# Kernel tuning notes

Hardware: AMD Instinct MI355X
Metric: run time of the kernel (lower is better)

Reference implementation:

```python
import jax, jax.numpy as jnp
import numpy as np

T = 16          # time_span
N = 128         # num_trajectory
D = 512         # embedding dim
TEMP = 0.1      # temperature
INF = 1000000000.0
M = 2 * N * T   # total rows of z (two views)


def setup_inputs() -> dict:
    key = jax.random.key(0)
    k1, k2 = jax.random.split(key)
    z = jax.random.normal(k1, (M, D), dtype=jnp.float32)
    done = jax.random.randint(k2, (T, N), 0, 2).astype(jnp.int32)  # [T, N] binary done flags
    return {"z": z, "done": done}


def _build_positive_mask(done):
    # done: [T, N] int -> transposed to [N, T] as in the torch code
    d = done.astype(jnp.float32).T  # [N, T]
    # Sequential rewrite loop is equivalent to:
    #   done_new[r,t] = 1 iff exists original done at p < t in row r AND orig done[r,t] == 0
    excl = jnp.cumsum(d, axis=1) - d  # exclusive cumsum along time
    d_new = jnp.where((excl > 0) & (d == 0), 1.0, 0.0)  # [N, T]
    done_vec = 1.0 - d_new.reshape(-1)  # [N*T]
    # block-diagonal temporal mask: same trajectory => 1
    traj = jnp.arange(N * T) // T
    block = (traj[:, None] == traj[None, :]).astype(jnp.float32)  # [NT, NT]
    done_mask = (done_vec[:, None] * done_vec[None, :]) * block
    done_mask = jnp.tile(done_mask, (2, 2))      # [M, M]
    temporal_mask = jnp.tile(block, (2, 2))      # [M, M]
    eye = jnp.eye(M, dtype=jnp.float32)
    positive_mask = (1.0 - done_mask) * (1.0 - temporal_mask) + eye
    return positive_mask, eye


def reference(z, done):
    positive_mask, eye = _build_positive_mask(done)
    # cosine similarity = normalize + GEMM (same math as broadcasted F.cosine_similarity)
    norms = jnp.maximum(jnp.linalg.norm(z, axis=-1, keepdims=True), 1e-8)
    zn = z / norms
    logits = (zn @ zn.T) / TEMP - eye * INF  # [M, M]
    log_probs = jax.nn.log_softmax(logits, axis=1)
    neg = 1.0 - positive_mask
    mean_log_prob = jnp.sum(neg * log_probs, axis=1) / jnp.sum(neg, axis=1)
    return -jnp.mean(mean_log_prob)
```

## Files before the change

### kernel.cpp

```cpp
#include <hip/hip_runtime.h>
#include <hip/hip_bf16.h>

typedef __bf16 bf16x8 __attribute__((ext_vector_type(8)));
typedef float f32x16 __attribute__((ext_vector_type(16)));
typedef unsigned int u32x4 __attribute__((ext_vector_type(4)));
typedef unsigned short u16;


__global__ void nrm_kernel(const float* __restrict__ z, u16* __restrict__ zn,
                           float* __restrict__ expsum, float* __restrict__ possum) {
    int row = blockIdx.x;
    int tid = threadIdx.x;
    float4 v = ((const float4*)(z + row * 512))[tid];
    float ss = v.x * v.x + v.y * v.y + v.z * v.z + v.w * v.w;
#pragma unroll
    for (int off = 32; off; off >>= 1) ss += __shfl_down(ss, off, 64);
    __shared__ float red[2];
    if ((tid & 63) == 0) red[tid >> 6] = ss;
    __syncthreads();
    float norm = fmaxf(sqrtf(red[0] + red[1]), 1e-8f);
    float sc = 1.0f / norm;
    __hip_bfloat16 b[4];
    b[0] = __float2bfloat16(v.x * sc);
    b[1] = __float2bfloat16(v.y * sc);
    b[2] = __float2bfloat16(v.z * sc);
    b[3] = __float2bfloat16(v.w * sc);
    uint2 p;
    __builtin_memcpy(&p, b, 8);
    ((uint2*)(zn + row * 512))[tid] = p;
    if (tid == 0) { expsum[row] = 0.f; possum[row] = 0.f; }
}

__global__ void pos_kernel(const u16* __restrict__ zn, float* __restrict__ possum) {
    int g = blockIdx.x;
    int l = threadIdx.x;
    int u = l & 31, h = l >> 5;
    int grow = (u < 16) ? (g * 16 + u) : (2048 + g * 16 + (u - 16));
    const u32x4* src = (const u32x4*)(zn + grow * 512);
    f32x16 acc = {};
#pragma unroll
    for (int kc = 0; kc < 32; ++kc) {
        bf16x8 f = __builtin_bit_cast(bf16x8, src[h + 2 * kc]);
        acc = __builtin_amdgcn_mfma_f32_32x32x16_bf16(f, f, acc, 0, 0, 0);
    }
#pragma unroll
    for (int r = 0; r < 16; ++r) {
        int rrow = (r & 3) + 8 * (r >> 2) + 4 * h;
        float v = (rrow == u) ? 0.f : acc[r];
        v += __shfl_xor(v, 1, 64);
        v += __shfl_xor(v, 2, 64);
        v += __shfl_xor(v, 4, 64);
        v += __shfl_xor(v, 8, 64);
        v += __shfl_xor(v, 16, 64);
        if (u == 0) {
            int gr = (rrow < 16) ? (g * 16 + rrow) : (2048 + g * 16 + (rrow - 16));
            possum[gr] = v * 10.0f;
        }
    }
}

__global__ __launch_bounds__(256, 2) void gemm_kernel(const u16* __restrict__ zn,
                                                      float* __restrict__ expsum) {
    __shared__ u16 Bt[32 * 520];
    int wave = threadIdx.x >> 6;
    int l = threadIdx.x & 63;
    int m = l & 31, h = l >> 5;
    int rowbase = blockIdx.x * 128 + wave * 32;
    int colchunk = blockIdx.y * 256;

    u32x4 a[32];
    const u32x4* arow = (const u32x4*)(zn + (rowbase + m) * 512);
#pragma unroll
    for (int kc = 0; kc < 32; ++kc) a[kc] = arow[h + 2 * kc];

    float expacc[16];
#pragma unroll
    for (int r = 0; r < 16; ++r) expacc[r] = 0.f;

    int c = threadIdx.x >> 3;
    int g0 = threadIdx.x & 7;

    for (int ct = 0; ct < 8; ++ct) {
        int colbase = colchunk + ct * 32;
        __syncthreads();
        const u32x4* src = (const u32x4*)(zn + (colbase + c) * 512);
        u32x4* dst = (u32x4*)(Bt + c * 520);
#pragma unroll
        for (int i = 0; i < 8; ++i) dst[g0 + 8 * i] = src[g0 + 8 * i];
        __syncthreads();

        f32x16 acc = {};
        const u32x4* brow = (const u32x4*)(Bt + m * 520);
#pragma unroll
        for (int kc = 0; kc < 32; ++kc) {
            bf16x8 bf = __builtin_bit_cast(bf16x8, brow[h + 2 * kc]);
            acc = __builtin_amdgcn_mfma_f32_32x32x16_bf16(
                __builtin_bit_cast(bf16x8, a[kc]), bf, acc, 0, 0, 0);
        }
        if (colbase == rowbase) {
#pragma unroll
            for (int r = 0; r < 16; ++r) {
                int rrow = (r & 3) + 8 * (r >> 2) + 4 * h;
                if (rrow != m) expacc[r] += __expf(acc[r] * 10.0f);
            }
        } else {
#pragma unroll
            for (int r = 0; r < 16; ++r) expacc[r] += __expf(acc[r] * 10.0f);
        }
    }
#pragma unroll
    for (int r = 0; r < 16; ++r) {
        float v = expacc[r];
        v += __shfl_xor(v, 1, 64);
        v += __shfl_xor(v, 2, 64);
        v += __shfl_xor(v, 4, 64);
        v += __shfl_xor(v, 8, 64);
        v += __shfl_xor(v, 16, 64);
        if (m == 0) {
            int rrow = (r & 3) + 8 * (r >> 2) + 4 * h;
            atomicAdd(&expsum[rowbase + rrow], v);
        }
    }
}

__global__ void fin_kernel(const float* __restrict__ expsum,
                           const float* __restrict__ possum, float* __restrict__ out) {
    int tid = threadIdx.x;
    float s = 0.f;
    for (int i = tid; i < 4096; i += 1024)
        s += __logf(expsum[i]) - possum[i] * (1.0f / 31.0f);
#pragma unroll
    for (int off = 32; off; off >>= 1) s += __shfl_down(s, off, 64);
    __shared__ float red[16];
    if ((tid & 63) == 0) red[tid >> 6] = s;
    __syncthreads();
    if (tid == 0) {
        float t = 0.f;
#pragma unroll
        for (int i = 0; i < 16; ++i) t += red[i];
        out[0] = t * (1.0f / 4096.0f);
    }
}

extern "C" void kernel_launch(void* const* d_in, const int* in_sizes, int n_in,
                              void* d_out, int out_size, void* d_ws, size_t ws_size,
                              hipStream_t stream) {
    const float* z = (const float*)d_in[0];
    u16* zn = (u16*)d_ws;
    float* expsum = (float*)((char*)d_ws + (4u << 20));
    float* possum = expsum + 4096;
    float* out = (float*)d_out;

    nrm_kernel<<<4096, 128, 0, stream>>>(z, zn, expsum, possum);
    pos_kernel<<<128, 64, 0, stream>>>(zn, possum);
    gemm_kernel<<<dim3(32, 16), 256, 0, stream>>>(zn, expsum);
    fin_kernel<<<1, 1024, 0, stream>>>(expsum, possum, out);
}
```

Measured before the change: 97.55 us.

## Exploit Gram symmetry with upper-triangular tiles and async double-buffered LDS loads

The GEMM now launches only the upper-triangular 128x128 block tiles (528 workgroups instead of 512 covering the full matrix, each with half the columns). Each off-diagonal tile contributes both row sums and column sums of exp(logits), with column sums added atomically. B tiles are streamed into a double-buffered, XOR-swizzled LDS buffer via global_load_lds async copies, and the K loop is split across two accumulators for more MFMA ILP. This roughly halves MFMA and exp work. In exchange it adds more atomics, per-block extra reduction work, and bf16 rounding that is now shared symmetrically.

After: 109.7 us. 1.12x slower.

```diff
diff --git a/kernel.cpp b/kernel.cpp
--- a/kernel.cpp
+++ b/kernel.cpp
@@ -6,6 +6,12 @@
 typedef unsigned int u32x4 __attribute__((ext_vector_type(4)));
 typedef unsigned short u16;
 
+
+__device__ inline void async_cp16(const u16* g, u16* l) {
+    __builtin_amdgcn_global_load_lds(
+        (const __attribute__((address_space(1))) unsigned int*)g,
+        (__attribute__((address_space(3))) unsigned int*)l, 16, 0, 0);
+}
 
 __global__ void nrm_kernel(const float* __restrict__ z, u16* __restrict__ zn,
                            float* __restrict__ expsum, float* __restrict__ possum) {
@@ -18,8 +24,7 @@
     __shared__ float red[2];
     if ((tid & 63) == 0) red[tid >> 6] = ss;
     __syncthreads();
-    float norm = fmaxf(sqrtf(red[0] + red[1]), 1e-8f);
-    float sc = 1.0f / norm;
+    float sc = 1.0f / fmaxf(sqrtf(red[0] + red[1]), 1e-8f);
     __hip_bfloat16 b[4];
     b[0] = __float2bfloat16(v.x * sc);
     b[1] = __float2bfloat16(v.y * sc);
@@ -61,15 +66,19 @@
 
 __global__ __launch_bounds__(256, 2) void gemm_kernel(const u16* __restrict__ zn,
                                                       float* __restrict__ expsum) {
-    __shared__ u16 Bt[32 * 520];
+    __shared__ u16 Bt[2][32 * 512];
     int wave = threadIdx.x >> 6;
     int l = threadIdx.x & 63;
     int m = l & 31, h = l >> 5;
-    int rowbase = blockIdx.x * 128 + wave * 32;
-    int colchunk = blockIdx.y * 256;
+
+    int t = blockIdx.x, i = 0;
+    while (t >= 32 - i) { t -= 32 - i; ++i; }
+    int j = i + t;
+    int rowbase = i * 128 + wave * 32;
+    bool diagwg = (i == j);
 
     u32x4 a[32];
-    const u32x4* arow = (const u32x4*)(zn + (rowbase + m) * 512);
+    const u32x4* arow = (const u32x4*)(zn + (size_t)(rowbase + m) * 512);
 #pragma unroll
     for (int kc = 0; kc < 32; ++kc) a[kc] = arow[h + 2 * kc];
 
@@ -77,35 +86,57 @@
 #pragma unroll
     for (int r = 0; r < 16; ++r) expacc[r] = 0.f;
 
-    int c = threadIdx.x >> 3;
-    int g0 = threadIdx.x & 7;
+    {
+        int colbase = j * 128;
+#pragma unroll
+        for (int it = 0; it < 8; ++it) {
+            int col = wave * 8 + it;
+            int s = col & 7;
+            async_cp16(zn + (size_t)(colbase + col) * 512 + ((l ^ s) * 8),
+                       &Bt[0][col * 512]);
+        }
+    }
 
-    for (int ct = 0; ct < 8; ++ct) {
-        int colbase = colchunk + ct * 32;
+    int sB = m & 7;
+    for (int ct = 0; ct < 4; ++ct) {
         __syncthreads();
-        const u32x4* src = (const u32x4*)(zn + (colbase + c) * 512);
-        u32x4* dst = (u32x4*)(Bt + c * 520);
+        if (ct < 3) {
+            int colbase = j * 128 + (ct + 1) * 32;
+            u16* dst = &Bt[(ct + 1) & 1][0];
 #pragma unroll
-        for (int i = 0; i < 8; ++i) dst[g0 + 8 * i] = src[g0 + 8 * i];
-        __syncthreads();
-
-        f32x16 acc = {};
-        const u32x4* brow = (const u32x4*)(Bt + m * 520);
+            for (int it = 0; it < 8; ++it) {
+                int col = wave * 8 + it;
+                int s = col & 7;
+                async_cp16(zn + (size_t)(colbase + col) * 512 + ((l ^ s) * 8),
+                           dst + col * 512);
+            }
+        }
+        const u16* bcol = &Bt[ct & 1][m * 512];
+        f32x16 acc0 = {}, acc1 = {};
 #pragma unroll
-        for (int kc = 0; kc < 32; ++kc) {
-            bf16x8 bf = __builtin_bit_cast(bf16x8, brow[h + 2 * kc]);
-            acc = __builtin_amdgcn_mfma_f32_32x32x16_bf16(
-                __builtin_bit_cast(bf16x8, a[kc]), bf, acc, 0, 0, 0);
+        for (int kc = 0; kc < 16; ++kc) {
+            bf16x8 b0 = *(const bf16x8*)(bcol + (((h + 4 * kc) ^ sB) * 8));
+            bf16x8 b1 = *(const bf16x8*)(bcol + (((h + 4 * kc + 2) ^ sB) * 8));
+            acc0 = __builtin_amdgcn_mfma_f32_32x32x16_bf16(
+                __builtin_bit_cast(bf16x8, a[2 * kc]), b0, acc0, 0, 0, 0);
+            acc1 = __builtin_amdgcn_mfma_f32_32x32x16_bf16(
+                __builtin_bit_cast(bf16x8, a[2 * kc + 1]), b1, acc1, 0, 0, 0);
         }
-        if (colbase == rowbase) {
+        int colbase = j * 128 + ct * 32;
+        bool diagtile = diagwg && (ct == wave);
+        float cs = 0.f;
 #pragma unroll
-            for (int r = 0; r < 16; ++r) {
-                int rrow = (r & 3) + 8 * (r >> 2) + 4 * h;
-                if (rrow != m) expacc[r] += __expf(acc[r] * 10.0f);
-            }
-        } else {
-#pragma unroll
-            for (int r = 0; r < 16; ++r) expacc[r] += __expf(acc[r] * 10.0f);
+        for (int r = 0; r < 16; ++r) {
+            int rrow = (r & 3) + 8 * (r >> 2) + 4 * h;
+            float e = (diagtile && rrow == m)
+                          ? 0.f
+                          : __expf((acc0[r] + acc1[r]) * 10.0f);
+            expacc[r] += e;
+            cs += e;
+        }
+        if (!diagwg) {
+            cs += __shfl_xor(cs, 32, 64);
+            if (h == 0) atomicAdd(&expsum[colbase + m], cs);
         }
     }
 #pragma unroll
@@ -153,6 +184,6 @@
 
     nrm_kernel<<<4096, 128, 0, stream>>>(z, zn, expsum, possum);
     pos_kernel<<<128, 64, 0, stream>>>(zn, possum);
-    gemm_kernel<<<dim3(32, 16), 256, 0, stream>>>(zn, expsum);
+    gemm_kernel<<<528, 256, 0, stream>>>(zn, expsum);
     fin_kernel<<<1, 1024, 0, stream>>>(expsum, possum, out);
 }
```
